# Kernel optimization log

Measured on AMD Instinct MI355X. Metric: run time of the kernel, lower is better.

## Reference

```python
import jax, jax.numpy as jnp
import numpy as np


def _shift(x, k):
    # roll time axis forward by k, zero-filling the first k steps
    if k == 0:
        return x
    return jnp.pad(x, ((0, 0), (k, 0), (0, 0)))[:, : x.shape[1]]


def _stu_conv(u, v, n):
    # u: (B,L,D), v: (L,K) spectral filters; non-tensordot branch of conv()
    B, L, D = u.shape
    K = v.shape[1]
    sgn = jnp.where(jnp.arange(L) % 2 == 1, -1.0, 1.0).astype(jnp.float32)[None, :, None, None]
    ue = jnp.broadcast_to(u[:, :, None, :], (B, L, K, D)).astype(jnp.float32)
    U = jnp.stack([ue, ue * sgn], axis=-1)                     # (B,L,K,D,2)
    Uf = jnp.fft.rfft(U, n=n, axis=1)
    vf = jnp.fft.rfft(v.astype(jnp.float32)[None, :, :, None, None], n=n, axis=1)
    Uc = jnp.fft.irfft(vf * Uf, n=n, axis=1)[:, :L]            # (B,L,K,D,2)
    U_plus = Uc[..., 0]
    U_minus = Uc[..., 1] * sgn
    return U_plus.astype(u.dtype), U_minus.astype(u.dtype)


def setup_inputs() -> dict:
    key = jax.random.key(0)
    ks = jax.random.split(key, 6)
    B, L, D, K, k_u, k_y = 2, 1024, 512, 16, 3, 2
    u = jax.random.normal(ks[0], (B, L, D), jnp.float32)
    filters = jax.random.normal(ks[1], (L, K), jnp.float32) / np.float32(np.sqrt(L))
    M_u = jax.random.normal(ks[2], (D, k_u, D), jnp.float32) * 0.01
    M_y = jax.random.normal(ks[3], (D, k_y, D), jnp.float32) * 0.01
    M_phi_plus = jax.random.normal(ks[4], (K, D, D), jnp.float32) * 0.01
    M_phi_minus = jax.random.normal(ks[5], (K, D, D), jnp.float32) * 0.01
    return {"u": u, "filters": filters, "M_u": M_u, "M_y": M_y,
            "M_phi_plus": M_phi_plus, "M_phi_minus": M_phi_minus}


def reference(u, filters, M_u, M_y, M_phi_plus, M_phi_minus):
    B, L, D = u.shape
    n = 1 << int(np.ceil(np.log2(2 * L - 1)))  # nearest power of two >= 2L-1
    k_u = M_u.shape[1]
    k_y = M_y.shape[1]

    # FFT-based long convolution with the +/- sign trick
    U_plus, U_minus = _stu_conv(u, filters, n)
    spectral = (jnp.einsum('blkd,kdo->blo', U_plus, M_phi_plus)
                + jnp.einsum('blkd,kdo->blo', U_minus, M_phi_minus))

    # input-AR term of compute_ar_strict: sum_j u[t+1-j] @ M_u[:, j-1].T (shifts 0..k_u-1)
    u_sh = jnp.stack([_shift(u, j - 1) for j in range(1, k_u + 1)], axis=1)  # (B,k_u,L,D)
    y_in = jnp.einsum('bjlf,ijf->bli', u_sh, M_u)

    z = spectral + y_in  # (B,L,D)

    # output-AR recurrence of compute_ar_strict as a scan
    def step(y_buf, z_t):
        y_t = z_t + jnp.einsum('bjf,djf->bd', y_buf, M_y)
        y_buf = jnp.concatenate([y_t[:, None], y_buf[:, :-1]], axis=1)
        return y_buf, y_t

    _, ys = jax.lax.scan(step, jnp.zeros((B, k_y, D), z.dtype), jnp.swapaxes(z, 0, 1))
    return jnp.swapaxes(ys, 0, 1)  # (B,L,D)
```

## Files before the change

### kernel.cpp

```cpp
#include <hip/hip_runtime.h>
#include <hip/hip_bf16.h>


using bf16 = __hip_bfloat16;
typedef __attribute__((ext_vector_type(8))) short bf16x8;
typedef __attribute__((ext_vector_type(4))) float f32x4;

#define B_   2
#define L_   1024
#define D_   512
#define K_   16
#define KT   17920
#define ROWS 2048
#define NTAP 6
#define PBLD 3584
#define SPLITD 16
#define SPLITR 12
#define ZBROWS 1032

#define WAIT_VM6 0x0F76
#define WAIT_VM0 0x0F70

__device__ __forceinline__ void gll16(const void* g, void* l) {
    __builtin_amdgcn_global_load_lds(
        (const __attribute__((address_space(1))) unsigned int*)g,
        (__attribute__((address_space(3))) unsigned int*)l, 16, 0, 0);
}

__global__ void prep_ew(const float* __restrict__ u, const float* __restrict__ fil,
                        const float* __restrict__ Mu, const float* __restrict__ My,
                        bf16* __restrict__ U, bf16* __restrict__ BT,
                        bf16* __restrict__ PB, bf16* __restrict__ W,
                        bf16* __restrict__ Myb) {
    int bid = blockIdx.x, tid = threadIdx.x;
    auto pack4 = [](float4 v) {
        ushort4 o; bf16 h;
        h = __float2bfloat16(v.x); o.x = *(unsigned short*)&h;
        h = __float2bfloat16(v.y); o.y = *(unsigned short*)&h;
        h = __float2bfloat16(v.z); o.z = *(unsigned short*)&h;
        h = __float2bfloat16(v.w); o.w = *(unsigned short*)&h;
        return o;
    };
    if (bid < 3072) {
        int e4 = bid * 256 + tid;
        int r = e4 / 384, rem = e4 % 384;
        int t = rem >> 7, f = (rem & 127) * 4;
        int b = r >> 10, l = r & 1023;
        float4 v = {0.f, 0.f, 0.f, 0.f};
        if (l >= t) v = *(const float4*)&u[((size_t)b * L_ + l - t) * D_ + f];
        *(ushort4*)&U[(size_t)r * KT + 16384 + t * 512 + f] = pack4(v);
    } else if (bid < 3840) {
        int e4 = (bid - 3072) * 256 + tid;
        int o = e4 / 384, tf4 = (e4 % 384) * 4;
        float4 v = *(const float4*)&Mu[(size_t)o * 1536 + tf4];
        *(ushort4*)&BT[(size_t)o * KT + 16384 + tf4] = pack4(v);
    } else if (bid < 4352) {
        int e4 = (bid - 3840) * 256 + tid;
        int n = e4 >> 8, c4 = (e4 & 255) * 4;
        float4 v;
        if (c4 < 512) {
            v.x = (n == c4) ? 1.f : 0.f;     v.y = (n == c4 + 1) ? 1.f : 0.f;
            v.z = (n == c4 + 2) ? 1.f : 0.f; v.w = (n == c4 + 3) ? 1.f : 0.f;
        } else v = *(const float4*)&My[(size_t)n * 1024 + (c4 - 512)];
        *(ushort4*)&PB[(size_t)n * PBLD + c4] = pack4(v);
    } else if (bid < 5120) {
        int tile = bid - 4352;
        int set = tile >> 8, rem = tile & 255;
        int k = rem >> 4, g = (rem >> 2) & 3, kb = rem & 3;
        for (int idx = tid; idx < 4096; idx += 256) {
            int i = idx >> 5, jp = idx & 31;
            int j = ((jp >> 3) ^ ((i >> 1) & 3)) * 8 + (jp & 7);
            int x = g * 128 + i - kb * 32 - j - (set == 2 ? 1 : 0);
            float v = 0.f;
            if (x >= 0) {
                int row = (set == 0) ? 2 * x : 2 * x + 1;
                v = fil[row * K_ + k];
            }
            W[(size_t)tile * 4096 + idx] = __float2bfloat16(v);
        }
    } else {
        int e4 = (bid - 5120) * 256 + tid;
        float4 v = *(const float4*)&My[(size_t)e4 * 4];
        *(ushort4*)&Myb[(size_t)e4 * 4] = pack4(v);
    }
}

__global__ void prep_tr(const float* __restrict__ Mp, const float* __restrict__ Mm,
                        const float* __restrict__ My, const float* __restrict__ u,
                        bf16* __restrict__ BT, bf16* __restrict__ BTT,
                        bf16* __restrict__ uPT) {
    __shared__ bf16 t[64][72];
    int zb = blockIdx.z;
    int col = threadIdx.x & 63, r0 = (threadIdx.x >> 6) * 16;
    if (zb < 32) {
        int dt = blockIdx.x * 64, ot = blockIdx.y * 64, c = zb;
        int k = c & 15;
        const float* sp = Mp + (size_t)k * D_ * D_;
        const float* sm = Mm + (size_t)k * D_ * D_;
        float sg = (c < 16) ? 1.f : -1.f;
        for (int i = 0; i < 16; ++i) {
            size_t o_ = (size_t)(dt + r0 + i) * D_ + ot + col;
            t[r0 + i][col] = __float2bfloat16(sp[o_] + sg * sm[o_]);
        }
        __syncthreads();
        for (int i = 0; i < 16; ++i)
            BT[(size_t)(ot + r0 + i) * KT + c * D_ + dt + col] = t[col][r0 + i];
    } else if (zb < 34) {
        int h = zb - 32;
        int dt = blockIdx.x * 64, ft = blockIdx.y * 64;
        for (int i = 0; i < 16; ++i)
            t[r0 + i][col] = __float2bfloat16(My[(size_t)(dt + r0 + i) * 1024 + (1 - h) * 512 + ft + col]);
        __syncthreads();
        for (int i = 0; i < 16; ++i)
            BTT[(size_t)(ft + r0 + i) * 1024 + h * 512 + dt + col] = t[col][r0 + i];
    } else {
        for (int it = 0; it < 4; ++it) {
            int b = it >> 1, p = it & 1;
            int mt = blockIdx.x * 64, dt = blockIdx.y * 64;
            __syncthreads();
            for (int i = 0; i < 16; ++i)
                t[r0 + i][col] = __float2bfloat16(u[((size_t)b * L_ + 2 * (mt + r0 + i) + p) * D_ + dt + col]);
            __syncthreads();
            for (int i = 0; i < 16; ++i)
                uPT[((size_t)it * 512 + dt + r0 + i) * 512 + mt + col] = t[col][r0 + i];
        }
    }
}

__device__ __forceinline__ void phi_body(
    const bf16* A, int lda, const bf16* BT, int ldb,
    bf16* out, int ldo, int klen, const bf16* add, int lad,
    int row0, int col0, bf16* sA, bf16* sB)
{
    const int tid = threadIdx.x, lane = tid & 63, wave = tid >> 6;
    const int wm = (wave & 1) * 64, wn = (wave >> 1) * 64;
    const int ml = lane & 15, q = lane >> 4;
    const int srow = lane >> 2, scol = (((lane & 3) ^ ((srow >> 1) & 3))) * 8;
    const int swz = ((ml >> 1) & 3);
    f32x4 acc[4][4] = {};

    for (int k = 0; k < klen; k += 32) {
        __syncthreads();
        #pragma unroll
        for (int repi = 0; repi < 2; ++repi) {
            int a = wave + repi * 4;
            gll16(A  + (size_t)(row0 + a * 16 + srow) * lda + k + scol, &sA[a * 512]);
            gll16(BT + (size_t)(col0 + a * 16 + srow) * ldb + k + scol, &sB[a * 512]);
        }
        __syncthreads();
        bf16x8 af[4], bfr[4];
        #pragma unroll
        for (int i = 0; i < 4; ++i)
            af[i] = *(const bf16x8*)&sA[(wm + i * 16 + ml) * 32 + (q ^ swz) * 8];
        #pragma unroll
        for (int j = 0; j < 4; ++j)
            bfr[j] = *(const bf16x8*)&sB[(wn + j * 16 + ml) * 32 + (q ^ swz) * 8];
        #pragma unroll
        for (int i = 0; i < 4; ++i)
            #pragma unroll
            for (int j = 0; j < 4; ++j)
                acc[i][j] = __builtin_amdgcn_mfma_f32_16x16x32_bf16(af[i], bfr[j], acc[i][j], 0, 0, 0);
    }
    #pragma unroll
    for (int i = 0; i < 4; ++i)
        #pragma unroll
        for (int j = 0; j < 4; ++j)
            #pragma unroll
            for (int reg = 0; reg < 4; ++reg) {
                int r = row0 + wm + i * 16 + q * 4 + reg;
                int cc = col0 + wn + j * 16 + ml;
                float v = acc[i][j][reg];
                if (add) v += __bfloat162float(add[(size_t)r * lad + cc]);
                out[(size_t)r * ldo + cc] = __float2bfloat16(v);
            }
}

__global__ void k_ztaps(const bf16* __restrict__ partD, float* __restrict__ z,
                        bf16* __restrict__ zbuf, bf16* PB, const bf16* BTT) {
    __shared__ bf16 sA[4096];
    __shared__ bf16 sB[4096];
    int bid = blockIdx.x;
    if (bid < 32) {
        int row0 = (bid & 3) * 128, col0 = (bid >> 2) * 128;
        phi_body(PB + 3 * 512, PBLD, BTT, 1024, PB + 5 * 512, PBLD, 1024,
                 nullptr, 0, row0, col0, sA, sB);
        return;
    }
    if (bid == 32) {
        ushort4 z4 = {0, 0, 0, 0};
        for (int i = 0; i < 8; ++i) {
            int e4 = i * 256 + threadIdx.x;
            int b = e4 >> 10, rem = e4 & 1023;
            int g = rem >> 7, c4 = (rem & 127) * 4;
            *(ushort4*)&zbuf[(size_t)(b * ZBROWS + g) * 512 + c4] = z4;
        }
        return;
    }
    int t = (bid - 33) * 256 + threadIdx.x;
    int r = t >> 7, f4 = (t & 127) * 4;
    const ushort4* p = (const ushort4*)partD;
    float4 s = {0.f, 0.f, 0.f, 0.f};
    #pragma unroll
    for (int c = 0; c < SPLITD; ++c) {
        ushort4 v = p[(size_t)c * (ROWS * D_ / 4) + t];
        s.x += __uint_as_float((unsigned)v.x << 16);
        s.y += __uint_as_float((unsigned)v.y << 16);
        s.z += __uint_as_float((unsigned)v.z << 16);
        s.w += __uint_as_float((unsigned)v.w << 16);
    }
    ((float4*)z)[t] = s;
    ushort4 zb4;
    { bf16 h;
      h = __float2bfloat16(s.x); zb4.x = *(unsigned short*)&h;
      h = __float2bfloat16(s.y); zb4.y = *(unsigned short*)&h;
      h = __float2bfloat16(s.z); zb4.z = *(unsigned short*)&h;
      h = __float2bfloat16(s.w); zb4.w = *(unsigned short*)&h; }
    int b = r >> 10, li = r & 1023;
    *(ushort4*)&zbuf[(size_t)(b * ZBROWS + 8 + li) * 512 + f4] = zb4;
}

__global__ void reduce_out(const float* __restrict__ z, const bf16* __restrict__ partR,
                           float* __restrict__ out) {
    int t = blockIdx.x * 256 + threadIdx.x;
    if (t >= ROWS * D_ / 4) return;
    float4 s = ((const float4*)z)[t];
    const ushort4* p = (const ushort4*)partR;
    #pragma unroll
    for (int c = 0; c < SPLITR; ++c) {
        ushort4 v = p[(size_t)c * (ROWS * D_ / 4) + t];
        s.x += __uint_as_float((unsigned)v.x << 16);
        s.y += __uint_as_float((unsigned)v.y << 16);
        s.z += __uint_as_float((unsigned)v.z << 16);
        s.w += __uint_as_float((unsigned)v.w << 16);
    }
    ((float4*)out)[t] = s;
}

__global__ __launch_bounds__(256, 2) void conv_misc(
    const bf16* __restrict__ W, const bf16* __restrict__ uPT,
    bf16* __restrict__ U,
    const bf16* PB, const bf16* BTT, const bf16* Myb)
{
    __shared__ bf16 sA[3][4096];
    __shared__ bf16 sB[3][8192];
    const int z = blockIdx.z;
    if (z < 6) {
        int which = z >> 1;
        int row0 = blockIdx.x * 128;
        int col0 = ((z & 1) * 2 + blockIdx.y) * 128;
        bf16* BTTw = (bf16*)BTT; bf16* PBw = (bf16*)PB;
        if (which == 0)
            phi_body(PB, PBLD, BTT, 1024, PBw + 2 * 512, PBLD, 1024,
                     nullptr, 0, row0, col0, &sA[0][0], &sB[0][0]);
        else if (which == 1)
            phi_body(BTT + 512, 1024, Myb + 512, 1024,
                     BTTw + (size_t)512 * 1024, 1024, 512,
                     nullptr, 0, row0, col0, &sA[0][0], &sB[0][0]);
        else
            phi_body(BTT + 512, 1024, Myb, 1024,
                     BTTw + (size_t)512 * 1024 + 512, 1024, 512,
                     BTT, 1024, row0, col0, &sA[0][0], &sB[0][0]);
        return;
    }
    const int zc = z - 6;
    const int mt = 3 - blockIdx.x, dt2 = blockIdx.y;
    const int t = zc & 3, b = (zc >> 2) & 1, k = zc >> 3;
    const int pb_ = t & 1;
    const int p = (t & 1) ^ (t >> 1);
    const int set = (t < 2) ? 0 : (t == 2 ? 1 : 2);
    const int ch = (t < 2) ? k : 16 + k;
    const int plane = b * 2 + pb_;
    const int tid = threadIdx.x, lane = tid & 63, wave = tid >> 6;
    const int wm = (wave & 1) * 64, wn = (wave >> 1) * 128;
    const int ml = lane & 15, q = lane >> 4;
    const int srow = lane >> 2, scol = (((lane & 3) ^ ((srow >> 1) & 3))) * 8;
    const int swz = ((ml >> 1) & 3);
    f32x4 acc[4][8] = {};
    const int n = (mt + 1) * 4;

    const bf16* bB[4];
    #pragma unroll
    for (int r = 0; r < 4; ++r)
        bB[r] = uPT + ((size_t)plane * 512 + dt2 * 256 + (wave + r * 4) * 16 + srow) * 512 + scol;
    const bf16* wbase = W + ((size_t)(set * 16 + k) * 16) * 4096;
    auto stage = [&](int s, int buf) {
        const bf16* wt = wbase + ((size_t)((mt - (s >> 2)) * 4 + (s & 3))) * 4096;
        gll16(wt + wave * 512 + lane * 8, &sA[buf][wave * 512]);
        gll16(wt + (wave + 4) * 512 + lane * 8, &sA[buf][(wave + 4) * 512]);
        #pragma unroll
        for (int r = 0; r < 4; ++r)
            gll16(bB[r] + s * 32, &sB[buf][(wave + r * 4) * 512]);
    };
    auto compute = [&](int c) {
        bf16x8 af[4], bfr[8];
        #pragma unroll
        for (int i = 0; i < 4; ++i)
            af[i] = *(const bf16x8*)&sA[c][(wm + i * 16 + ml) * 32 + (q ^ swz) * 8];
        #pragma unroll
        for (int j = 0; j < 8; ++j)
            bfr[j] = *(const bf16x8*)&sB[c][(wn + j * 16 + ml) * 32 + (q ^ swz) * 8];
        #pragma unroll
        for (int i = 0; i < 4; ++i)
            #pragma unroll
            for (int j = 0; j < 8; ++j)
                acc[i][j] = __builtin_amdgcn_mfma_f32_16x16x32_bf16(af[i], bfr[j], acc[i][j], 0, 0, 0);
    };
    stage(0, 0); stage(1, 1);
    int c = 0, nb = 2;
    for (int i = 0; i < n - 1; ++i) {
        __builtin_amdgcn_s_waitcnt(WAIT_VM6);
        __builtin_amdgcn_s_barrier();
        if (i + 2 < n) stage(i + 2, nb);
        compute(c);
        c = (c == 2) ? 0 : c + 1; nb = (nb == 2) ? 0 : nb + 1;
    }
    __builtin_amdgcn_s_waitcnt(WAIT_VM0);
    __builtin_amdgcn_s_barrier();
    compute(c);

    #pragma unroll
    for (int i = 0; i < 4; ++i)
        #pragma unroll
        for (int j = 0; j < 8; ++j)
            #pragma unroll
            for (int reg = 0; reg < 4; ++reg) {
                int m = mt * 128 + wm + i * 16 + q * 4 + reg;
                int l = 2 * m + p;
                int d = dt2 * 256 + wn + j * 16 + ml;
                U[(size_t)(b * L_ + l) * KT + ch * 512 + d] = __float2bfloat16(acc[i][j][reg]);
            }
}

__global__ __launch_bounds__(256, 2) void gemm_k(
    const bf16* __restrict__ A, int lda, int k_chunk,
    const bf16* __restrict__ BT, int ldb,
    bf16* __restrict__ part,
    const bf16* __restrict__ zbuf,
    int swzgrid, const bf16* PB, const bf16* BTT)
{
    __shared__ bf16 sA[3][4096];
    __shared__ bf16 sB[3][8192];
    int row0, col0, zz;
    if (swzgrid) {
        int id = blockIdx.x;
        if (id < 32) {
            int r0_ = (id & 3) * 128, c0_ = (id >> 2) * 128;
            phi_body(PB + 512, PBLD, BTT, 1024, (bf16*)PB + 3 * 512, PBLD, 1024,
                     nullptr, 0, r0_, c0_, &sA[0][0], &sB[0][0]);
            return;
        }
        id -= 32;
        int xcd = id & 7, n_ = id >> 3;
        zz = xcd + 8 * (n_ >> 5);
        int rem = n_ & 31;
        row0 = (rem >> 1) * 128;
        col0 = (rem & 1) * 256;
    } else {
        row0 = blockIdx.x * 128; col0 = blockIdx.y * 256; zz = blockIdx.z;
    }
    const int tid = threadIdx.x, lane = tid & 63, wave = tid >> 6;
    const int wm = (wave & 1) * 64, wn = (wave >> 1) * 128;
    const int ml = lane & 15, q = lane >> 4;
    const int srow = lane >> 2, scol = (((lane & 3) ^ ((srow >> 1) & 3))) * 8;
    const int swz = ((ml >> 1) & 3);
    f32x4 acc[4][8] = {};

    const bf16* Abase; int alda, n, k0;
    if (zbuf) {
        int s = 1 + (zz >> 1), koff = (zz & 1) * 256;
        int b = row0 >> 10, li0 = row0 & 1023;
        Abase = zbuf + ((size_t)(b * ZBROWS + 8 + li0 - s)) * 512 + koff;
        alda = 512; n = 8; k0 = zz * 256;
    } else {
        Abase = A + (size_t)row0 * lda + (size_t)zz * k_chunk;
        alda = lda; n = k_chunk >> 5; k0 = zz * k_chunk;
    }
    const bf16* bA0 = Abase + (size_t)(wave * 16 + srow) * alda + scol;
    const bf16* bA1 = Abase + (size_t)((wave + 4) * 16 + srow) * alda + scol;
    const bf16* bB[4];
    #pragma unroll
    for (int r = 0; r < 4; ++r)
        bB[r] = BT + (size_t)(col0 + (wave + r * 4) * 16 + srow) * ldb + k0 + scol;

    auto stage = [&](int s, int buf) {
        gll16(bA0 + s * 32, &sA[buf][wave * 512]);
        gll16(bA1 + s * 32, &sA[buf][(wave + 4) * 512]);
        #pragma unroll
        for (int r = 0; r < 4; ++r)
            gll16(bB[r] + s * 32, &sB[buf][(wave + r * 4) * 512]);
    };
    auto compute = [&](int c) {
        bf16x8 af[4], bfr[8];
        #pragma unroll
        for (int i = 0; i < 4; ++i)
            af[i] = *(const bf16x8*)&sA[c][(wm + i * 16 + ml) * 32 + (q ^ swz) * 8];
        #pragma unroll
        for (int j = 0; j < 8; ++j)
            bfr[j] = *(const bf16x8*)&sB[c][(wn + j * 16 + ml) * 32 + (q ^ swz) * 8];
        #pragma unroll
        for (int i = 0; i < 4; ++i)
            #pragma unroll
            for (int j = 0; j < 8; ++j)
                acc[i][j] = __builtin_amdgcn_mfma_f32_16x16x32_bf16(af[i], bfr[j], acc[i][j], 0, 0, 0);
    };
    stage(0, 0); stage(1, 1);
    int c = 0, nb = 2;
    for (int i = 0; i < n - 1; ++i) {
        __builtin_amdgcn_s_waitcnt(WAIT_VM6);
        __builtin_amdgcn_s_barrier();
        if (i + 2 < n) stage(i + 2, nb);
        compute(c);
        c = (c == 2) ? 0 : c + 1; nb = (nb == 2) ? 0 : nb + 1;
    }
    __builtin_amdgcn_s_waitcnt(WAIT_VM0);
    __builtin_amdgcn_s_barrier();
    compute(c);

    bf16* o = part + (size_t)zz * ROWS * D_;
    #pragma unroll
    for (int i = 0; i < 4; ++i)
        #pragma unroll
        for (int j = 0; j < 8; ++j)
            #pragma unroll
            for (int reg = 0; reg < 4; ++reg) {
                int r = row0 + wm + i * 16 + q * 4 + reg;
                int cc = col0 + wn + j * 16 + ml;
                o[(size_t)r * D_ + cc] = __float2bfloat16(acc[i][j][reg]);
            }
}

extern "C" void kernel_launch(void* const* d_in, const int* in_sizes, int n_in,
                              void* d_out, int out_size, void* d_ws, size_t ws_size,
                              hipStream_t stream) {
    const float* u   = (const float*)d_in[0];
    const float* fil = (const float*)d_in[1];
    const float* Mu  = (const float*)d_in[2];
    const float* My  = (const float*)d_in[3];
    const float* Mp  = (const float*)d_in[4];
    const float* Mm  = (const float*)d_in[5];
    float* out = (float*)d_out;

    char* ws = (char*)d_ws;
    size_t off = 0;
    auto alloc = [&](size_t bytes) { void* p = ws + off; off = (off + bytes + 255) & ~(size_t)255; return p; };
    bf16*  U    = (bf16*) alloc((size_t)ROWS * KT * 2);
    bf16*  BT   = (bf16*) alloc((size_t)512 * KT * 2);
    bf16*  PB   = (bf16*) alloc((size_t)512 * PBLD * 2);
    bf16*  BTT  = (bf16*) alloc((size_t)1024 * 1024 * 2);
    bf16*  Myb  = (bf16*) alloc((size_t)512 * 1024 * 2);
    float* z    = (float*)alloc((size_t)ROWS * D_ * 4);
    bf16*  zb   = (bf16*) alloc((size_t)B_ * ZBROWS * 512 * 2);
    char*  region = (char*)alloc((size_t)SPLITD * ROWS * D_ * 2);
    bf16*  W    = (bf16*)region;
    bf16*  uPT  = (bf16*)(region + (size_t)768 * 4096 * 2);
    bf16*  partD = (bf16*)region;
    bf16*  partR = (bf16*)region;

    prep_ew<<<5632, 256, 0, stream>>>(u, fil, Mu, My, U, BT, PB, W, Myb);
    prep_tr<<<dim3(8, 8, 35), 256, 0, stream>>>(Mp, Mm, My, u, BT, BTT, uPT);

    conv_misc<<<dim3(4, 2, 134), 256, 0, stream>>>(W, uPT, U, PB, BTT, Myb);

    gemm_k<<<576, 256, 0, stream>>>(U, KT, KT / SPLITD, BT, KT, partD,
                                    nullptr, 1, PB, BTT);

    k_ztaps<<<1057, 256, 0, stream>>>(partD, z, zb, PB, BTT);

    gemm_k<<<dim3(16, 2, SPLITR), 256, 0, stream>>>(nullptr, 0, 256,
                                                    PB + 512, PBLD, partR,
                                                    zb, 0, nullptr, nullptr);

    reduce_out<<<(ROWS * D_ / 4 + 255) / 256, 256, 0, stream>>>(z, partR, out);
}
```

Before: 282.8 us.

## Merge prep kernels, shrink conv tiles, halve output-AR split-K

The two prep kernels are fused into one launch, with the transpose work appended as extra blocks. The conv GEMM in conv_misc drops from 128x256 to 128x128 tiles, with less shared memory and a launch bound allowing three blocks per CU, and the grid is reshaped to match. The final output-AR GEMM uses half as many K splits, so reduce_out has fewer partials to read, and the first gemm_k grid shrinks by 32 blocks. The aim is less launch overhead, better occupancy and less partial-sum traffic, at the cost of more per-block work in the final GEMM and changed first-GEMM scheduling that may leave some tile work uncovered.

```diff
diff --git a/kernel.cpp b/kernel.cpp
--- a/kernel.cpp
+++ b/kernel.cpp
@@ -15,10 +15,11 @@
 #define NTAP 6
 #define PBLD 3584
 #define SPLITD 16
-#define SPLITR 12
+#define SPLITR 6
 #define ZBROWS 1032
 
 #define WAIT_VM6 0x0F76
+#define WAIT_VM4 0x0F74
 #define WAIT_VM0 0x0F70
 
 __device__ __forceinline__ void gll16(const void* g, void* l) {
@@ -27,11 +28,14 @@
         (__attribute__((address_space(3))) unsigned int*)l, 16, 0, 0);
 }
 
-__global__ void prep_ew(const float* __restrict__ u, const float* __restrict__ fil,
-                        const float* __restrict__ Mu, const float* __restrict__ My,
-                        bf16* __restrict__ U, bf16* __restrict__ BT,
-                        bf16* __restrict__ PB, bf16* __restrict__ W,
-                        bf16* __restrict__ Myb) {
+__global__ void prep_all(const float* __restrict__ u, const float* __restrict__ fil,
+                         const float* __restrict__ Mu, const float* __restrict__ My,
+                         const float* __restrict__ Mp, const float* __restrict__ Mm,
+                         bf16* __restrict__ U, bf16* __restrict__ BT,
+                         bf16* __restrict__ PB, bf16* __restrict__ W,
+                         bf16* __restrict__ Myb, bf16* __restrict__ BTT,
+                         bf16* __restrict__ uPT) {
+    __shared__ bf16 t[64][72];
     int bid = blockIdx.x, tid = threadIdx.x;
     auto pack4 = [](float4 v) {
         ushort4 o; bf16 h;
@@ -44,11 +48,11 @@
     if (bid < 3072) {
         int e4 = bid * 256 + tid;
         int r = e4 / 384, rem = e4 % 384;
-        int t = rem >> 7, f = (rem & 127) * 4;
+        int tt = rem >> 7, f = (rem & 127) * 4;
         int b = r >> 10, l = r & 1023;
         float4 v = {0.f, 0.f, 0.f, 0.f};
-        if (l >= t) v = *(const float4*)&u[((size_t)b * L_ + l - t) * D_ + f];
-        *(ushort4*)&U[(size_t)r * KT + 16384 + t * 512 + f] = pack4(v);
+        if (l >= tt) v = *(const float4*)&u[((size_t)b * L_ + l - tt) * D_ + f];
+        *(ushort4*)&U[(size_t)r * KT + 16384 + tt * 512 + f] = pack4(v);
     } else if (bid < 3840) {
         int e4 = (bid - 3072) * 256 + tid;
         int o = e4 / 384, tf4 = (e4 % 384) * 4;
@@ -78,51 +82,47 @@
             }
             W[(size_t)tile * 4096 + idx] = __float2bfloat16(v);
         }
-    } else {
+    } else if (bid < 5632) {
         int e4 = (bid - 5120) * 256 + tid;
         float4 v = *(const float4*)&My[(size_t)e4 * 4];
         *(ushort4*)&Myb[(size_t)e4 * 4] = pack4(v);
-    }
-}
-
-__global__ void prep_tr(const float* __restrict__ Mp, const float* __restrict__ Mm,
-                        const float* __restrict__ My, const float* __restrict__ u,
-                        bf16* __restrict__ BT, bf16* __restrict__ BTT,
-                        bf16* __restrict__ uPT) {
-    __shared__ bf16 t[64][72];
-    int zb = blockIdx.z;
-    int col = threadIdx.x & 63, r0 = (threadIdx.x >> 6) * 16;
-    if (zb < 32) {
-        int dt = blockIdx.x * 64, ot = blockIdx.y * 64, c = zb;
-        int k = c & 15;
-        const float* sp = Mp + (size_t)k * D_ * D_;
-        const float* sm = Mm + (size_t)k * D_ * D_;
-        float sg = (c < 16) ? 1.f : -1.f;
-        for (int i = 0; i < 16; ++i) {
-            size_t o_ = (size_t)(dt + r0 + i) * D_ + ot + col;
-            t[r0 + i][col] = __float2bfloat16(sp[o_] + sg * sm[o_]);
-        }
-        __syncthreads();
-        for (int i = 0; i < 16; ++i)
-            BT[(size_t)(ot + r0 + i) * KT + c * D_ + dt + col] = t[col][r0 + i];
-    } else if (zb < 34) {
-        int h = zb - 32;
-        int dt = blockIdx.x * 64, ft = blockIdx.y * 64;
-        for (int i = 0; i < 16; ++i)
-            t[r0 + i][col] = __float2bfloat16(My[(size_t)(dt + r0 + i) * 1024 + (1 - h) * 512 + ft + col]);
-        __syncthreads();
-        for (int i = 0; i < 16; ++i)
-            BTT[(size_t)(ft + r0 + i) * 1024 + h * 512 + dt + col] = t[col][r0 + i];
     } else {
-        for (int it = 0; it < 4; ++it) {
-            int b = it >> 1, p = it & 1;
-            int mt = blockIdx.x * 64, dt = blockIdx.y * 64;
+        int tt = bid - 5632;
+        int zb = tt >> 6, rem = tt & 63;
+        int bx = rem & 7, by = rem >> 3;
+        int col = tid & 63, r0 = (tid >> 6) * 16;
+        if (zb < 32) {
+            int dt = bx * 64, ot = by * 64, c = zb;
+            int k = c & 15;
+            const float* sp = Mp + (size_t)k * D_ * D_;
+            const float* sm = Mm + (size_t)k * D_ * D_;
+            float sg = (c < 16) ? 1.f : -1.f;
+            for (int i = 0; i < 16; ++i) {
+                size_t o_ = (size_t)(dt + r0 + i) * D_ + ot + col;
+                t[r0 + i][col] = __float2bfloat16(sp[o_] + sg * sm[o_]);
+            }
             __syncthreads();
             for (int i = 0; i < 16; ++i)
-                t[r0 + i][col] = __float2bfloat16(u[((size_t)b * L_ + 2 * (mt + r0 + i) + p) * D_ + dt + col]);
+                BT[(size_t)(ot + r0 + i) * KT + c * D_ + dt + col] = t[col][r0 + i];
+        } else if (zb < 34) {
+            int h = zb - 32;
+            int dt = bx * 64, ft = by * 64;
+            for (int i = 0; i < 16; ++i)
+                t[r0 + i][col] = __float2bfloat16(My[(size_t)(dt + r0 + i) * 1024 + (1 - h) * 512 + ft + col]);
             __syncthreads();
             for (int i = 0; i < 16; ++i)
-                uPT[((size_t)it * 512 + dt + r0 + i) * 512 + mt + col] = t[col][r0 + i];
+                BTT[(size_t)(ft + r0 + i) * 1024 + h * 512 + dt + col] = t[col][r0 + i];
+        } else {
+            for (int it = 0; it < 4; ++it) {
+                int b = it >> 1, p = it & 1;
+                int mt = bx * 64, dt = by * 64;
+                __syncthreads();
+                for (int i = 0; i < 16; ++i)
+                    t[r0 + i][col] = __float2bfloat16(u[((size_t)b * L_ + 2 * (mt + r0 + i) + p) * D_ + dt + col]);
+                __syncthreads();
+                for (int i = 0; i < 16; ++i)
+                    uPT[((size_t)it * 512 + dt + r0 + i) * 512 + mt + col] = t[col][r0 + i];
+            }
         }
     }
 }
@@ -236,23 +236,21 @@
     ((float4*)out)[t] = s;
 }
 
-__global__ __launch_bounds__(256, 2) void conv_misc(
+__global__ __launch_bounds__(256, 3) void conv_misc(
     const bf16* __restrict__ W, const bf16* __restrict__ uPT,
     bf16* __restrict__ U,
     const bf16* PB, const bf16* BTT, const bf16* Myb)
 {
     __shared__ bf16 sA[3][4096];
-    __shared__ bf16 sB[3][8192];
+    __shared__ bf16 sB[3][4096];
     const int z = blockIdx.z;
-    if (z < 6) {
-        int which = z >> 1;
-        int row0 = blockIdx.x * 128;
-        int col0 = ((z & 1) * 2 + blockIdx.y) * 128;
+    if (z < 3) {
+        int row0 = blockIdx.x * 128, col0 = blockIdx.y * 128;
         bf16* BTTw = (bf16*)BTT; bf16* PBw = (bf16*)PB;
-        if (which == 0)
+        if (z == 0)
             phi_body(PB, PBLD, BTT, 1024, PBw + 2 * 512, PBLD, 1024,
                      nullptr, 0, row0, col0, &sA[0][0], &sB[0][0]);
-        else if (which == 1)
+        else if (z == 1)
             phi_body(BTT + 512, 1024, Myb + 512, 1024,
                      BTTw + (size_t)512 * 1024, 1024, 512,
                      nullptr, 0, row0, col0, &sA[0][0], &sB[0][0]);
@@ -262,8 +260,8 @@
                      BTT, 1024, row0, col0, &sA[0][0], &sB[0][0]);
         return;
     }
-    const int zc = z - 6;
-    const int mt = 3 - blockIdx.x, dt2 = blockIdx.y;
+    const int zc = z - 3;
+    const int mt = 3 - blockIdx.x, dt = blockIdx.y * 128;
     const int t = zc & 3, b = (zc >> 2) & 1, k = zc >> 3;
     const int pb_ = t & 1;
     const int p = (t & 1) ^ (t >> 1);
@@ -271,44 +269,41 @@
     const int ch = (t < 2) ? k : 16 + k;
     const int plane = b * 2 + pb_;
     const int tid = threadIdx.x, lane = tid & 63, wave = tid >> 6;
-    const int wm = (wave & 1) * 64, wn = (wave >> 1) * 128;
+    const int wm = (wave & 1) * 64, wn = (wave >> 1) * 64;
     const int ml = lane & 15, q = lane >> 4;
     const int srow = lane >> 2, scol = (((lane & 3) ^ ((srow >> 1) & 3))) * 8;
     const int swz = ((ml >> 1) & 3);
-    f32x4 acc[4][8] = {};
+    f32x4 acc[4][4] = {};
     const int n = (mt + 1) * 4;
 
-    const bf16* bB[4];
-    #pragma unroll
-    for (int r = 0; r < 4; ++r)
-        bB[r] = uPT + ((size_t)plane * 512 + dt2 * 256 + (wave + r * 4) * 16 + srow) * 512 + scol;
+    const bf16* bB0 = uPT + ((size_t)plane * 512 + dt + wave * 16       + srow) * 512 + scol;
+    const bf16* bB1 = uPT + ((size_t)plane * 512 + dt + (wave + 4) * 16 + srow) * 512 + scol;
     const bf16* wbase = W + ((size_t)(set * 16 + k) * 16) * 4096;
     auto stage = [&](int s, int buf) {
         const bf16* wt = wbase + ((size_t)((mt - (s >> 2)) * 4 + (s & 3))) * 4096;
         gll16(wt + wave * 512 + lane * 8, &sA[buf][wave * 512]);
         gll16(wt + (wave + 4) * 512 + lane * 8, &sA[buf][(wave + 4) * 512]);
-        #pragma unroll
-        for (int r = 0; r < 4; ++r)
-            gll16(bB[r] + s * 32, &sB[buf][(wave + r * 4) * 512]);
+        gll16(bB0 + s * 32, &sB[buf][wave * 512]);
+        gll16(bB1 + s * 32, &sB[buf][(wave + 4) * 512]);
     };
     auto compute = [&](int c) {
-        bf16x8 af[4], bfr[8];
+        bf16x8 af[4], bfr[4];
         #pragma unroll
         for (int i = 0; i < 4; ++i)
             af[i] = *(const bf16x8*)&sA[c][(wm + i * 16 + ml) * 32 + (q ^ swz) * 8];
         #pragma unroll
-        for (int j = 0; j < 8; ++j)
+        for (int j = 0; j < 4; ++j)
             bfr[j] = *(const bf16x8*)&sB[c][(wn + j * 16 + ml) * 32 + (q ^ swz) * 8];
         #pragma unroll
         for (int i = 0; i < 4; ++i)
             #pragma unroll
-            for (int j = 0; j < 8; ++j)
+            for (int j = 0; j < 4; ++j)
                 acc[i][j] = __builtin_amdgcn_mfma_f32_16x16x32_bf16(af[i], bfr[j], acc[i][j], 0, 0, 0);
     };
     stage(0, 0); stage(1, 1);
     int c = 0, nb = 2;
     for (int i = 0; i < n - 1; ++i) {
-        __builtin_amdgcn_s_waitcnt(WAIT_VM6);
+        __builtin_amdgcn_s_waitcnt(WAIT_VM4);
         __builtin_amdgcn_s_barrier();
         if (i + 2 < n) stage(i + 2, nb);
         compute(c);
@@ -321,12 +316,12 @@
     #pragma unroll
     for (int i = 0; i < 4; ++i)
         #pragma unroll
-        for (int j = 0; j < 8; ++j)
+        for (int j = 0; j < 4; ++j)
             #pragma unroll
             for (int reg = 0; reg < 4; ++reg) {
                 int m = mt * 128 + wm + i * 16 + q * 4 + reg;
                 int l = 2 * m + p;
-                int d = dt2 * 256 + wn + j * 16 + ml;
+                int d = dt + wn + j * 16 + ml;
                 U[(size_t)(b * L_ + l) * KT + ch * 512 + d] = __float2bfloat16(acc[i][j][reg]);
             }
 }
@@ -367,10 +362,10 @@
 
     const bf16* Abase; int alda, n, k0;
     if (zbuf) {
-        int s = 1 + (zz >> 1), koff = (zz & 1) * 256;
+        int s = 1 + zz;
         int b = row0 >> 10, li0 = row0 & 1023;
-        Abase = zbuf + ((size_t)(b * ZBROWS + 8 + li0 - s)) * 512 + koff;
-        alda = 512; n = 8; k0 = zz * 256;
+        Abase = zbuf + ((size_t)(b * ZBROWS + 8 + li0 - s)) * 512;
+        alda = 512; n = 16; k0 = zz * 512;
     } else {
         Abase = A + (size_t)row0 * lda + (size_t)zz * k_chunk;
         alda = lda; n = k_chunk >> 5; k0 = zz * k_chunk;
@@ -456,17 +451,17 @@
     bf16*  partD = (bf16*)region;
     bf16*  partR = (bf16*)region;
 
-    prep_ew<<<5632, 256, 0, stream>>>(u, fil, Mu, My, U, BT, PB, W, Myb);
-    prep_tr<<<dim3(8, 8, 35), 256, 0, stream>>>(Mp, Mm, My, u, BT, BTT, uPT);
-
-    conv_misc<<<dim3(4, 2, 134), 256, 0, stream>>>(W, uPT, U, PB, BTT, Myb);
-
-    gemm_k<<<576, 256, 0, stream>>>(U, KT, KT / SPLITD, BT, KT, partD,
+    prep_all<<<7872, 256, 0, stream>>>(u, fil, Mu, My, Mp, Mm,
+                                       U, BT, PB, W, Myb, BTT, uPT);
+
+    conv_misc<<<dim3(4, 4, 131), 256, 0, stream>>>(W, uPT, U, PB, BTT, Myb);
+
+    gemm_k<<<544, 256, 0, stream>>>(U, KT, KT / SPLITD, BT, KT, partD,
                                     nullptr, 1, PB, BTT);
 
     k_ztaps<<<1057, 256, 0, stream>>>(partD, z, zb, PB, BTT);
 
-    gemm_k<<<dim3(16, 2, SPLITR), 256, 0, stream>>>(nullptr, 0, 256,
+    gemm_k<<<dim3(16, 2, SPLITR), 256, 0, stream>>>(nullptr, 0, 512,
                                                     PB + 512, PBLD, partR,
                                                     zb, 0, nullptr, nullptr);
 
```

New measurement: 253.4 us. -10.4%, faster.
